# Kernel optimization log

Hardware: AMD Instinct MI355X
Metric: run time of the kernel (lower is better)

Reference implementation:

```python
import jax, jax.numpy as jnp
import numpy as np

N_NODES = 50000
N_EDGES = 1600000
D_FEAT = 128
EPS = 1e-12  # matches F.normalize clamp_min eps


def setup_inputs() -> dict:
    key = jax.random.key(0)
    k1, k2 = jax.random.split(key)
    x = jax.random.normal(k1, (N_NODES, D_FEAT), dtype=jnp.float32)
    beta = jnp.ones((1,), dtype=jnp.float32)  # AGNNConv learnable scalar, init 1.0
    edge_index = jax.random.randint(k2, (2, N_EDGES), 0, N_NODES, dtype=jnp.int64)
    return {"x": x, "beta": beta, "edge_index": edge_index}


def reference(x, beta, edge_index):
    N = x.shape[0]
    # AGNNConv default add_self_loops=True
    loop = jnp.arange(N, dtype=edge_index.dtype)
    src = jnp.concatenate([edge_index[0], loop])  # j (source / message sender)
    dst = jnp.concatenate([edge_index[1], loop])  # i (target / aggregator)

    # cosine-similarity attention logits per edge, scaled by beta
    xn = x * jax.lax.rsqrt(jnp.maximum(jnp.sum(x * x, axis=-1, keepdims=True), EPS * EPS))
    logits = beta[0] * jnp.sum(xn[src] * xn[dst], axis=-1)  # [E+N]

    # segment softmax over incoming edges of each target node
    m = jax.ops.segment_max(logits, dst, num_segments=N)
    m = jax.lax.stop_gradient(m)
    e = jnp.exp(logits - m[dst])
    s = jax.ops.segment_sum(e, dst, num_segments=N)
    alpha = e / s[dst]  # self-loops guarantee s > 0

    # scatter-aggregate messages alpha_e * x_src
    out = jax.ops.segment_sum(alpha[:, None] * x[src], dst, num_segments=N)

    # wrapper: activation (relu); normalization=False; dropout p=0 -> identity
    return jax.nn.relu(out)
```

## Files before the change

### kernel.cpp

```cpp
#include <hip/hip_runtime.h>

#define NN 50000
#define NE 1600000
#define DF 128
#define NB 1250
#define BSZ 40
#define CAP 1664
#define NWGP 512
#define CHKP 3125
#define NBN 12500

static __device__ __forceinline__ float bflo(unsigned int u) {
    unsigned int v = u << 16; float f; __builtin_memcpy(&f, &v, 4); return f;
}
static __device__ __forceinline__ float bfhi(unsigned int u) {
    unsigned int v = u & 0xFFFF0000u; float f; __builtin_memcpy(&f, &v, 4); return f;
}
static __device__ __forceinline__ unsigned int f2bf(float f) {
    unsigned int u; __builtin_memcpy(&u, &f, 4);
    u += 0x7FFFu + ((u >> 16) & 1u);
    return u >> 16;
}

static __device__ __forceinline__ int block_excl_scan(int v, int t, int* wsum4) {
    int lane = t & 63, wv = t >> 6;
    int s = v;
    #pragma unroll
    for (int off = 1; off < 64; off <<= 1) {
        int u = __shfl_up(s, off);
        if (lane >= off) s += u;
    }
    if (lane == 63) wsum4[wv] = s;
    __syncthreads();
    int add = 0;
    #pragma unroll
    for (int w = 0; w < 4; ++w) add += (w < wv) ? wsum4[w] : 0;
    __syncthreads();
    return s + add - v;
}

__global__ __launch_bounds__(256)
void k_norm_part(const float* __restrict__ x,
                 const int* __restrict__ ei,
                 unsigned int* __restrict__ xn_bf,
                 float* __restrict__ norm,
                 unsigned int* __restrict__ descG,
                 unsigned int* __restrict__ pairs) {
    __shared__ int wsum4[4];
    __shared__ int cntL[NB];
    __shared__ int offL[NB];
    __shared__ unsigned int stg[CHKP];
    if (blockIdx.x >= NWGP) {
        int node = ((blockIdx.x - NWGP) * 256 + threadIdx.x) >> 6;
        int lane = threadIdx.x & 63;
        float2 v = ((const float2*)(x + (size_t)node * DF))[lane];
        float ss = v.x * v.x + v.y * v.y;
        #pragma unroll
        for (int m = 1; m < 64; m <<= 1) ss += __shfl_xor(ss, m);
        float rinv = rsqrtf(fmaxf(ss, 1e-24f));
        xn_bf[(size_t)node * 64 + lane] = (f2bf(v.y * rinv) << 16) | f2bf(v.x * rinv);
        if (lane == 0) norm[node] = ss * rinv;
        return;
    }
    int wg = blockIdx.x, t = threadIdx.x;
    const int* srcp = ei + wg * CHKP;
    const int* dstp = ei + NE + wg * CHKP;
    for (int i = t; i < NB; i += 256) cntL[i] = 0;
    __syncthreads();
    for (int i = t; i < CHKP; i += 256) atomicAdd(&cntL[dstp[i] / BSZ], 1);
    __syncthreads();
    {
        int base = t * 5;
        int loc[5];
        int s = 0;
        #pragma unroll
        for (int q = 0; q < 5; ++q) {
            int idx = base + q;
            int v = (idx < NB) ? cntL[idx] : 0;
            loc[q] = s;
            s += v;
        }
        int ex = block_excl_scan(s, t, wsum4);
        #pragma unroll
        for (int q = 0; q < 5; ++q) {
            int idx = base + q;
            if (idx < NB) offL[idx] = ex + loc[q];
        }
    }
    __syncthreads();
    for (int i = t; i < NB; i += 256)
        descG[(size_t)wg * NB + i] = ((unsigned int)offL[i] << 16) | (unsigned int)cntL[i];
    __syncthreads();
    for (int i = t; i < CHKP; i += 256) {
        int src = srcp[i];
        int dst = dstp[i];
        int b = dst / BSZ;
        int pos = atomicAdd(&offL[b], 1);
        stg[pos] = ((unsigned int)(dst - b * BSZ) << 16) | (unsigned int)src;
    }
    __syncthreads();
    unsigned int* chunk = pairs + (size_t)wg * CHKP;
    for (int i = t; i < CHKP; i += 256) chunk[i] = stg[i];
}

__global__ __launch_bounds__(256)
void k_build(const float* __restrict__ norm,
             const unsigned int* __restrict__ descG,
             const unsigned int* __restrict__ pairs,
             unsigned int* __restrict__ colG,
             int2* __restrict__ rp2) {
    __shared__ int wsum4[4];
    __shared__ int lenS[NWGP], offS[NWGP], rbase[NWGP];
    __shared__ unsigned int rawL[CAP];
    __shared__ unsigned int colL[CAP];
    __shared__ int hist[BSZ];
    __shared__ int rp[BSZ + 1];
    __shared__ int tot0, stotal;
    int b = blockIdx.x, t = threadIdx.x;

    unsigned int d0 = descG[(size_t)t * NB + b];
    unsigned int d1 = descG[(size_t)(t + 256) * NB + b];
    int len0 = (int)(d0 & 0xFFFFu), off0 = (int)(d0 >> 16);
    int len1 = (int)(d1 & 0xFFFFu), off1 = (int)(d1 >> 16);
    int rb0 = block_excl_scan(len0, t, wsum4);
    if (t == 255) tot0 = rb0 + len0;
    int ex1 = block_excl_scan(len1, t, wsum4);
    int rb1 = tot0 + ex1;
    if (t == 255) stotal = rb1 + len1;
    lenS[t] = len0;        offS[t] = off0;        rbase[t] = rb0;
    lenS[t + 256] = len1;  offS[t + 256] = off1;  rbase[t + 256] = rb1;
    if (t < BSZ) hist[t] = 0;
    __syncthreads();
    int cnt = stotal;
    if (cnt > CAP) cnt = CAP;

    int g16 = t >> 4, l16 = t & 15;
    for (int r = g16; r < NWGP; r += 16) {
        int len = lenS[r];
        int rb = rbase[r];
        const unsigned int* sp = pairs + (size_t)r * CHKP + offS[r];
        for (int q = l16; q < len; q += 16) {
            int pos = rb + q;
            if (pos < CAP) rawL[pos] = sp[q];
        }
    }
    __syncthreads();
    for (int i = t; i < cnt; i += 256) atomicAdd(&hist[rawL[i] >> 16], 1);
    __syncthreads();
    if (t < 64) {
        int v = (t < BSZ) ? hist[t] : 0;
        int s = v;
        #pragma unroll
        for (int off = 1; off < 64; off <<= 1) {
            int u = __shfl_up(s, off);
            if (t >= off) s += u;
        }
        if (t < BSZ) { rp[t + 1] = s; hist[t] = s - v; }
        if (t == 0) rp[0] = 0;
    }
    __syncthreads();
    for (int i = t; i < cnt; i += 256) {
        unsigned int p = rawL[i];
        unsigned int src = p & 0xFFFFu;
        int pos = atomicAdd(&hist[p >> 16], 1);
        colL[pos] = (f2bf(norm[src]) << 16) | src;
    }
    __syncthreads();
    int base = b * CAP;
    for (int i = t; i < cnt; i += 256) colG[base + i] = colL[i];
    if (t < BSZ) {
        int2 v; v.x = base + rp[t]; v.y = base + rp[t + 1];
        rp2[b * BSZ + t] = v;
    }
}

__global__ __launch_bounds__(256)
void k_gather(const unsigned int* __restrict__ xn_bf,
              const float* __restrict__ norm,
              const int2* __restrict__ rp2,
              const unsigned int* __restrict__ colG,
              const float* __restrict__ beta_p,
              float* __restrict__ out) {
    int node = (blockIdx.x * blockDim.x + threadIdx.x) >> 6;
    int lane = threadIdx.x & 63;
    if (node >= NN) return;
    int j = lane & 15;
    int g = lane >> 4;
    float beta = beta_p[0];
    float c = -fabsf(beta);

    uint4 du = ((const uint4*)(xn_bf + (size_t)node * 64))[j];
    float xd[8];
    #pragma unroll
    for (int q = 0; q < 4; ++q) {
        unsigned int u = (&du.x)[q];
        xd[2 * q]     = bflo(u);
        xd[2 * q + 1] = bfhi(u);
    }

    float acc[8] = {0.f, 0.f, 0.f, 0.f, 0.f, 0.f, 0.f, 0.f};
    float ssum = 0.f;
    int2 rr = rp2[node];
    int b0 = rr.x, b1 = rr.y;

    int k = b0 + g;
    int kA = (k     < b1) ? k     : 0;
    int kB = (k + 4 < b1) ? k + 4 : 0;
    unsigned int pA = colG[kA];
    unsigned int pB = colG[kB];
    uint4 rA = ((const uint4*)(xn_bf + (size_t)(pA & 0xFFFFu) * 64))[j];
    uint4 rB = ((const uint4*)(xn_bf + (size_t)(pB & 0xFFFFu) * 64))[j];

    for (; k < b1; k += 8) {
        int kC = (k +  8 < b1) ? k +  8 : 0;
        int kD = (k + 12 < b1) ? k + 12 : 0;
        unsigned int pC = colG[kC];
        unsigned int pD = colG[kD];
        uint4 rC = ((const uint4*)(xn_bf + (size_t)(pC & 0xFFFFu) * 64))[j];
        uint4 rD = ((const uint4*)(xn_bf + (size_t)(pD & 0xFFFFu) * 64))[j];
        {
            float xs[8];
            #pragma unroll
            for (int q = 0; q < 4; ++q) {
                unsigned int u = (&rA.x)[q];
                xs[2 * q]     = bflo(u);
                xs[2 * q + 1] = bfhi(u);
            }
            float dot = 0.f;
            #pragma unroll
            for (int q = 0; q < 8; ++q) dot = fmaf(xd[q], xs[q], dot);
            dot += __shfl_xor(dot, 1);
            dot += __shfl_xor(dot, 2);
            dot += __shfl_xor(dot, 4);
            dot += __shfl_xor(dot, 8);
            float e = __expf(fmaf(beta, dot, c));
            ssum += e;
            float wgt = e * bfhi(pA);
            #pragma unroll
            for (int q = 0; q < 8; ++q) acc[q] = fmaf(wgt, xs[q], acc[q]);
        }
        {
            float xs[8];
            #pragma unroll
            for (int q = 0; q < 4; ++q) {
                unsigned int u = (&rB.x)[q];
                xs[2 * q]     = bflo(u);
                xs[2 * q + 1] = bfhi(u);
            }
            float dot = 0.f;
            #pragma unroll
            for (int q = 0; q < 8; ++q) dot = fmaf(xd[q], xs[q], dot);
            dot += __shfl_xor(dot, 1);
            dot += __shfl_xor(dot, 2);
            dot += __shfl_xor(dot, 4);
            dot += __shfl_xor(dot, 8);
            float e = __expf(fmaf(beta, dot, c));
            e = (k + 4 < b1) ? e : 0.f;
            ssum += e;
            float wgt = e * bfhi(pB);
            #pragma unroll
            for (int q = 0; q < 8; ++q) acc[q] = fmaf(wgt, xs[q], acc[q]);
        }
        pA = pC; pB = pD; rA = rC; rB = rD;
    }

    ssum += __shfl_xor(ssum, 16);
    ssum += __shfl_xor(ssum, 32);
    #pragma unroll
    for (int q = 0; q < 8; ++q) {
        acc[q] += __shfl_xor(acc[q], 16);
        acc[q] += __shfl_xor(acc[q], 32);
    }
    float e_self = __expf(beta + c);
    ssum += e_self;
    float wsl = e_self * norm[node];
    #pragma unroll
    for (int q = 0; q < 8; ++q) acc[q] = fmaf(wsl, xd[q], acc[q]);

    if (g == 0) {
        float inv = 1.0f / ssum;
        float4 o0, o1;
        o0.x = fmaxf(0.f, acc[0] * inv); o0.y = fmaxf(0.f, acc[1] * inv);
        o0.z = fmaxf(0.f, acc[2] * inv); o0.w = fmaxf(0.f, acc[3] * inv);
        o1.x = fmaxf(0.f, acc[4] * inv); o1.y = fmaxf(0.f, acc[5] * inv);
        o1.z = fmaxf(0.f, acc[6] * inv); o1.w = fmaxf(0.f, acc[7] * inv);
        float4* op = (float4*)(out + (size_t)node * DF + 8 * j);
        op[0] = o0;
        op[1] = o1;
    }
}

extern "C" void kernel_launch(void* const* d_in, const int* in_sizes, int n_in,
                              void* d_out, int out_size, void* d_ws, size_t ws_size,
                              hipStream_t stream) {
    const float* x    = (const float*)d_in[0];
    const float* beta = (const float*)d_in[1];
    const int*   ei   = (const int*)d_in[2];
    float*       out  = (float*)d_out;

    char* ws = (char*)d_ws;
    unsigned int* xn_bf = (unsigned int*)ws;
    float* norm = (float*)(ws + 12800000);
    unsigned int* descG = (unsigned int*)(ws + 13000000);
    unsigned int* pairs = (unsigned int*)(ws + 15560000);
    unsigned int* colG  = (unsigned int*)(ws + 21960000);
    int2* rp2 = (int2*)(ws + 30280000);

    k_norm_part<<<NWGP + NBN, 256, 0, stream>>>(x, ei, xn_bf, norm, descG, pairs);
    k_build    <<<NB,         256, 0, stream>>>(norm, descG, pairs, colG, rp2);
    k_gather   <<<(NN * 64 + 255) / 256, 256, 0, stream>>>(xn_bf, norm, rp2, colG, beta, out);
}
```

Measured before the change: 167.0 us.

## Fuse CSR build with gather and widen partition kernel to 512 threads

Merges the bucket build kernel and the gather/softmax kernel so each 40-node bucket's sorted column list stays in shared memory and is consumed directly, dropping the colG/rp2 global round trip and one launch. The partition kernel moves to 512-thread blocks with a 512-wide scan, and the normalization path processes two nodes per wave using float4 loads. The trade-off is that the gather now runs with only 1250 blocks of 4 waves, each looping over 10 nodes, so there is less parallelism and latency hiding for the random row fetches.

```diff
diff --git a/kernel.cpp b/kernel.cpp
--- a/kernel.cpp
+++ b/kernel.cpp
@@ -8,7 +8,7 @@
 #define CAP 1664
 #define NWGP 512
 #define CHKP 3125
-#define NBN 12500
+#define NBF 3125
 
 static __device__ __forceinline__ float bflo(unsigned int u) {
     unsigned int v = u << 16; float f; __builtin_memcpy(&f, &v, 4); return f;
@@ -22,7 +22,7 @@
     return u >> 16;
 }
 
-static __device__ __forceinline__ int block_excl_scan(int v, int t, int* wsum4) {
+static __device__ __forceinline__ int block_excl_scan512(int v, int t, int* wsum8) {
     int lane = t & 63, wv = t >> 6;
     int s = v;
     #pragma unroll
@@ -30,6 +30,23 @@
         int u = __shfl_up(s, off);
         if (lane >= off) s += u;
     }
+    if (lane == 63) wsum8[wv] = s;
+    __syncthreads();
+    int add = 0;
+    #pragma unroll
+    for (int w = 0; w < 8; ++w) add += (w < wv) ? wsum8[w] : 0;
+    __syncthreads();
+    return s + add - v;
+}
+
+static __device__ __forceinline__ int block_excl_scan256(int v, int t, int* wsum4) {
+    int lane = t & 63, wv = t >> 6;
+    int s = v;
+    #pragma unroll
+    for (int off = 1; off < 64; off <<= 1) {
+        int u = __shfl_up(s, off);
+        if (lane >= off) s += u;
+    }
     if (lane == 63) wsum4[wv] = s;
     __syncthreads();
     int add = 0;
@@ -39,59 +56,66 @@
     return s + add - v;
 }
 
-__global__ __launch_bounds__(256)
+__global__ __launch_bounds__(512)
 void k_norm_part(const float* __restrict__ x,
                  const int* __restrict__ ei,
                  unsigned int* __restrict__ xn_bf,
                  float* __restrict__ norm,
                  unsigned int* __restrict__ descG,
                  unsigned int* __restrict__ pairs) {
-    __shared__ int wsum4[4];
+    __shared__ int wsum8[8];
     __shared__ int cntL[NB];
     __shared__ int offL[NB];
     __shared__ unsigned int stg[CHKP];
+    int t = threadIdx.x;
     if (blockIdx.x >= NWGP) {
-        int node = ((blockIdx.x - NWGP) * 256 + threadIdx.x) >> 6;
-        int lane = threadIdx.x & 63;
-        float2 v = ((const float2*)(x + (size_t)node * DF))[lane];
-        float ss = v.x * v.x + v.y * v.y;
-        #pragma unroll
-        for (int m = 1; m < 64; m <<= 1) ss += __shfl_xor(ss, m);
+        int nbid = blockIdx.x - NWGP;
+        int l32 = t & 31;
+        int node = nbid * 16 + ((t >> 6) << 1) + ((t & 63) >> 5);
+        float4 v = ((const float4*)(x + (size_t)node * DF))[l32];
+        float ss = v.x * v.x + v.y * v.y + v.z * v.z + v.w * v.w;
+        #pragma unroll
+        for (int m = 1; m < 32; m <<= 1) ss += __shfl_xor(ss, m);
         float rinv = rsqrtf(fmaxf(ss, 1e-24f));
-        xn_bf[(size_t)node * 64 + lane] = (f2bf(v.y * rinv) << 16) | f2bf(v.x * rinv);
-        if (lane == 0) norm[node] = ss * rinv;
+        uint2 p;
+        p.x = (f2bf(v.y * rinv) << 16) | f2bf(v.x * rinv);
+        p.y = (f2bf(v.w * rinv) << 16) | f2bf(v.z * rinv);
+        ((uint2*)(xn_bf + (size_t)node * 64))[l32] = p;
+        if (l32 == 0) norm[node] = ss * rinv;
         return;
     }
-    int wg = blockIdx.x, t = threadIdx.x;
+    int wg = blockIdx.x;
     const int* srcp = ei + wg * CHKP;
     const int* dstp = ei + NE + wg * CHKP;
-    for (int i = t; i < NB; i += 256) cntL[i] = 0;
-    __syncthreads();
-    for (int i = t; i < CHKP; i += 256) atomicAdd(&cntL[dstp[i] / BSZ], 1);
+    for (int i = t; i < NB; i += 512) cntL[i] = 0;
+    __syncthreads();
+    #pragma unroll 4
+    for (int i = t; i < CHKP; i += 512) atomicAdd(&cntL[dstp[i] / BSZ], 1);
     __syncthreads();
     {
-        int base = t * 5;
-        int loc[5];
+        int base = t * 3;
+        int loc[3];
         int s = 0;
         #pragma unroll
-        for (int q = 0; q < 5; ++q) {
+        for (int q = 0; q < 3; ++q) {
             int idx = base + q;
             int v = (idx < NB) ? cntL[idx] : 0;
             loc[q] = s;
             s += v;
         }
-        int ex = block_excl_scan(s, t, wsum4);
-        #pragma unroll
-        for (int q = 0; q < 5; ++q) {
+        int ex = block_excl_scan512(s, t, wsum8);
+        #pragma unroll
+        for (int q = 0; q < 3; ++q) {
             int idx = base + q;
             if (idx < NB) offL[idx] = ex + loc[q];
         }
     }
     __syncthreads();
-    for (int i = t; i < NB; i += 256)
+    for (int i = t; i < NB; i += 512)
         descG[(size_t)wg * NB + i] = ((unsigned int)offL[i] << 16) | (unsigned int)cntL[i];
     __syncthreads();
-    for (int i = t; i < CHKP; i += 256) {
+    #pragma unroll 2
+    for (int i = t; i < CHKP; i += 512) {
         int src = srcp[i];
         int dst = dstp[i];
         int b = dst / BSZ;
@@ -100,15 +124,17 @@
     }
     __syncthreads();
     unsigned int* chunk = pairs + (size_t)wg * CHKP;
-    for (int i = t; i < CHKP; i += 256) chunk[i] = stg[i];
+    #pragma unroll 4
+    for (int i = t; i < CHKP; i += 512) chunk[i] = stg[i];
 }
 
 __global__ __launch_bounds__(256)
-void k_build(const float* __restrict__ norm,
-             const unsigned int* __restrict__ descG,
-             const unsigned int* __restrict__ pairs,
-             unsigned int* __restrict__ colG,
-             int2* __restrict__ rp2) {
+void k_build_gather(const unsigned int* __restrict__ xn_bf,
+                    const float* __restrict__ norm,
+                    const unsigned int* __restrict__ descG,
+                    const unsigned int* __restrict__ pairs,
+                    const float* __restrict__ beta_p,
+                    float* __restrict__ out) {
     __shared__ int wsum4[4];
     __shared__ int lenS[NWGP], offS[NWGP], rbase[NWGP];
     __shared__ unsigned int rawL[CAP];
@@ -122,9 +148,9 @@
     unsigned int d1 = descG[(size_t)(t + 256) * NB + b];
     int len0 = (int)(d0 & 0xFFFFu), off0 = (int)(d0 >> 16);
     int len1 = (int)(d1 & 0xFFFFu), off1 = (int)(d1 >> 16);
-    int rb0 = block_excl_scan(len0, t, wsum4);
+    int rb0 = block_excl_scan256(len0, t, wsum4);
     if (t == 255) tot0 = rb0 + len0;
-    int ex1 = block_excl_scan(len1, t, wsum4);
+    int ex1 = block_excl_scan256(len1, t, wsum4);
     int rb1 = tot0 + ex1;
     if (t == 255) stotal = rb1 + len1;
     lenS[t] = len0;        offS[t] = off0;        rbase[t] = rb0;
@@ -166,127 +192,112 @@
         colL[pos] = (f2bf(norm[src]) << 16) | src;
     }
     __syncthreads();
-    int base = b * CAP;
-    for (int i = t; i < cnt; i += 256) colG[base + i] = colL[i];
-    if (t < BSZ) {
-        int2 v; v.x = base + rp[t]; v.y = base + rp[t + 1];
-        rp2[b * BSZ + t] = v;
-    }
-}
-
-__global__ __launch_bounds__(256)
-void k_gather(const unsigned int* __restrict__ xn_bf,
-              const float* __restrict__ norm,
-              const int2* __restrict__ rp2,
-              const unsigned int* __restrict__ colG,
-              const float* __restrict__ beta_p,
-              float* __restrict__ out) {
-    int node = (blockIdx.x * blockDim.x + threadIdx.x) >> 6;
-    int lane = threadIdx.x & 63;
-    if (node >= NN) return;
+
+    int lane = t & 63;
+    int w = t >> 6;
     int j = lane & 15;
     int g = lane >> 4;
     float beta = beta_p[0];
     float c = -fabsf(beta);
-
-    uint4 du = ((const uint4*)(xn_bf + (size_t)node * 64))[j];
-    float xd[8];
-    #pragma unroll
-    for (int q = 0; q < 4; ++q) {
-        unsigned int u = (&du.x)[q];
-        xd[2 * q]     = bflo(u);
-        xd[2 * q + 1] = bfhi(u);
-    }
-
-    float acc[8] = {0.f, 0.f, 0.f, 0.f, 0.f, 0.f, 0.f, 0.f};
-    float ssum = 0.f;
-    int2 rr = rp2[node];
-    int b0 = rr.x, b1 = rr.y;
-
-    int k = b0 + g;
-    int kA = (k     < b1) ? k     : 0;
-    int kB = (k + 4 < b1) ? k + 4 : 0;
-    unsigned int pA = colG[kA];
-    unsigned int pB = colG[kB];
-    uint4 rA = ((const uint4*)(xn_bf + (size_t)(pA & 0xFFFFu) * 64))[j];
-    uint4 rB = ((const uint4*)(xn_bf + (size_t)(pB & 0xFFFFu) * 64))[j];
-
-    for (; k < b1; k += 8) {
-        int kC = (k +  8 < b1) ? k +  8 : 0;
-        int kD = (k + 12 < b1) ? k + 12 : 0;
-        unsigned int pC = colG[kC];
-        unsigned int pD = colG[kD];
-        uint4 rC = ((const uint4*)(xn_bf + (size_t)(pC & 0xFFFFu) * 64))[j];
-        uint4 rD = ((const uint4*)(xn_bf + (size_t)(pD & 0xFFFFu) * 64))[j];
-        {
-            float xs[8];
-            #pragma unroll
-            for (int q = 0; q < 4; ++q) {
-                unsigned int u = (&rA.x)[q];
-                xs[2 * q]     = bflo(u);
-                xs[2 * q + 1] = bfhi(u);
+    for (int ln = w; ln < BSZ; ln += 4) {
+        int node = b * BSZ + ln;
+        uint4 du = ((const uint4*)(xn_bf + (size_t)node * 64))[j];
+        float xd[8];
+        #pragma unroll
+        for (int q = 0; q < 4; ++q) {
+            unsigned int u = (&du.x)[q];
+            xd[2 * q]     = bflo(u);
+            xd[2 * q + 1] = bfhi(u);
+        }
+        float acc[8] = {0.f, 0.f, 0.f, 0.f, 0.f, 0.f, 0.f, 0.f};
+        float ssum = 0.f;
+        int b0 = rp[ln], b1 = rp[ln + 1];
+
+        int k = b0 + g;
+        int kA = (k     < b1) ? k     : 0;
+        int kB = (k + 4 < b1) ? k + 4 : 0;
+        unsigned int pA = colL[kA];
+        unsigned int pB = colL[kB];
+        uint4 rA = ((const uint4*)(xn_bf + (size_t)(pA & 0xFFFFu) * 64))[j];
+        uint4 rB = ((const uint4*)(xn_bf + (size_t)(pB & 0xFFFFu) * 64))[j];
+
+        for (; k < b1; k += 8) {
+            int kC = (k +  8 < b1) ? k +  8 : 0;
+            int kD = (k + 12 < b1) ? k + 12 : 0;
+            unsigned int pC = colL[kC];
+            unsigned int pD = colL[kD];
+            uint4 rC = ((const uint4*)(xn_bf + (size_t)(pC & 0xFFFFu) * 64))[j];
+            uint4 rD = ((const uint4*)(xn_bf + (size_t)(pD & 0xFFFFu) * 64))[j];
+            {
+                float xs[8];
+                #pragma unroll
+                for (int q = 0; q < 4; ++q) {
+                    unsigned int u = (&rA.x)[q];
+                    xs[2 * q]     = bflo(u);
+                    xs[2 * q + 1] = bfhi(u);
+                }
+                float dot = 0.f;
+                #pragma unroll
+                for (int q = 0; q < 8; ++q) dot = fmaf(xd[q], xs[q], dot);
+                dot += __shfl_xor(dot, 1);
+                dot += __shfl_xor(dot, 2);
+                dot += __shfl_xor(dot, 4);
+                dot += __shfl_xor(dot, 8);
+                float e = __expf(fmaf(beta, dot, c));
+                ssum += e;
+                float wgt = e * bfhi(pA);
+                #pragma unroll
+                for (int q = 0; q < 8; ++q) acc[q] = fmaf(wgt, xs[q], acc[q]);
             }
-            float dot = 0.f;
-            #pragma unroll
-            for (int q = 0; q < 8; ++q) dot = fmaf(xd[q], xs[q], dot);
-            dot += __shfl_xor(dot, 1);
-            dot += __shfl_xor(dot, 2);
-            dot += __shfl_xor(dot, 4);
-            dot += __shfl_xor(dot, 8);
-            float e = __expf(fmaf(beta, dot, c));
-            ssum += e;
-            float wgt = e * bfhi(pA);
-            #pragma unroll
-            for (int q = 0; q < 8; ++q) acc[q] = fmaf(wgt, xs[q], acc[q]);
-        }
-        {
-            float xs[8];
-            #pragma unroll
-            for (int q = 0; q < 4; ++q) {
-                unsigned int u = (&rB.x)[q];
-                xs[2 * q]     = bflo(u);
-                xs[2 * q + 1] = bfhi(u);
+            {
+                float xs[8];
+                #pragma unroll
+                for (int q = 0; q < 4; ++q) {
+                    unsigned int u = (&rB.x)[q];
+                    xs[2 * q]     = bflo(u);
+                    xs[2 * q + 1] = bfhi(u);
+                }
+                float dot = 0.f;
+                #pragma unroll
+                for (int q = 0; q < 8; ++q) dot = fmaf(xd[q], xs[q], dot);
+                dot += __shfl_xor(dot, 1);
+                dot += __shfl_xor(dot, 2);
+                dot += __shfl_xor(dot, 4);
+                dot += __shfl_xor(dot, 8);
+                float e = __expf(fmaf(beta, dot, c));
+                e = (k + 4 < b1) ? e : 0.f;
+                ssum += e;
+                float wgt = e * bfhi(pB);
+                #pragma unroll
+                for (int q = 0; q < 8; ++q) acc[q] = fmaf(wgt, xs[q], acc[q]);
             }
-            float dot = 0.f;
-            #pragma unroll
-            for (int q = 0; q < 8; ++q) dot = fmaf(xd[q], xs[q], dot);
-            dot += __shfl_xor(dot, 1);
-            dot += __shfl_xor(dot, 2);
-            dot += __shfl_xor(dot, 4);
-            dot += __shfl_xor(dot, 8);
-            float e = __expf(fmaf(beta, dot, c));
-            e = (k + 4 < b1) ? e : 0.f;
-            ssum += e;
-            float wgt = e * bfhi(pB);
-            #pragma unroll
-            for (int q = 0; q < 8; ++q) acc[q] = fmaf(wgt, xs[q], acc[q]);
-        }
-        pA = pC; pB = pD; rA = rC; rB = rD;
-    }
-
-    ssum += __shfl_xor(ssum, 16);
-    ssum += __shfl_xor(ssum, 32);
-    #pragma unroll
-    for (int q = 0; q < 8; ++q) {
-        acc[q] += __shfl_xor(acc[q], 16);
-        acc[q] += __shfl_xor(acc[q], 32);
-    }
-    float e_self = __expf(beta + c);
-    ssum += e_self;
-    float wsl = e_self * norm[node];
-    #pragma unroll
-    for (int q = 0; q < 8; ++q) acc[q] = fmaf(wsl, xd[q], acc[q]);
-
-    if (g == 0) {
-        float inv = 1.0f / ssum;
-        float4 o0, o1;
-        o0.x = fmaxf(0.f, acc[0] * inv); o0.y = fmaxf(0.f, acc[1] * inv);
-        o0.z = fmaxf(0.f, acc[2] * inv); o0.w = fmaxf(0.f, acc[3] * inv);
-        o1.x = fmaxf(0.f, acc[4] * inv); o1.y = fmaxf(0.f, acc[5] * inv);
-        o1.z = fmaxf(0.f, acc[6] * inv); o1.w = fmaxf(0.f, acc[7] * inv);
-        float4* op = (float4*)(out + (size_t)node * DF + 8 * j);
-        op[0] = o0;
-        op[1] = o1;
+            pA = pC; pB = pD; rA = rC; rB = rD;
+        }
+
+        ssum += __shfl_xor(ssum, 16);
+        ssum += __shfl_xor(ssum, 32);
+        #pragma unroll
+        for (int q = 0; q < 8; ++q) {
+            acc[q] += __shfl_xor(acc[q], 16);
+            acc[q] += __shfl_xor(acc[q], 32);
+        }
+        float e_self = __expf(beta + c);
+        ssum += e_self;
+        float wsl = e_self * norm[node];
+        #pragma unroll
+        for (int q = 0; q < 8; ++q) acc[q] = fmaf(wsl, xd[q], acc[q]);
+
+        if (g == 0) {
+            float inv = 1.0f / ssum;
+            float4 o0, o1;
+            o0.x = fmaxf(0.f, acc[0] * inv); o0.y = fmaxf(0.f, acc[1] * inv);
+            o0.z = fmaxf(0.f, acc[2] * inv); o0.w = fmaxf(0.f, acc[3] * inv);
+            o1.x = fmaxf(0.f, acc[4] * inv); o1.y = fmaxf(0.f, acc[5] * inv);
+            o1.z = fmaxf(0.f, acc[6] * inv); o1.w = fmaxf(0.f, acc[7] * inv);
+            float4* op = (float4*)(out + (size_t)node * DF + 8 * j);
+            op[0] = o0;
+            op[1] = o1;
+        }
     }
 }
 
@@ -303,10 +314,7 @@
     float* norm = (float*)(ws + 12800000);
     unsigned int* descG = (unsigned int*)(ws + 13000000);
     unsigned int* pairs = (unsigned int*)(ws + 15560000);
-    unsigned int* colG  = (unsigned int*)(ws + 21960000);
-    int2* rp2 = (int2*)(ws + 30280000);
-
-    k_norm_part<<<NWGP + NBN, 256, 0, stream>>>(x, ei, xn_bf, norm, descG, pairs);
-    k_build    <<<NB,         256, 0, stream>>>(norm, descG, pairs, colG, rp2);
-    k_gather   <<<(NN * 64 + 255) / 256, 256, 0, stream>>>(xn_bf, norm, rp2, colG, beta, out);
-}
+
+    k_norm_part  <<<NWGP + NBF, 512, 0, stream>>>(x, ei, xn_bf, norm, descG, pairs);
+    k_build_gather<<<NB,        256, 0, stream>>>(xn_bf, norm, descG, pairs, beta, out);
+}
```

Result: faster. 162.1 us (-2.9%).
